# Kernel tuning notes

Measured on AMD Instinct MI355X. Metric: run time of the kernel, lower is better.

The kernel has to match this reference:

```python
import jax, jax.numpy as jnp
import numpy as np

IH, IW, HEADS, DIM_HEAD = 32, 32, 8, 48
N = IH * IW
SCALE = DIM_HEAD ** -0.5
EPS = 1e-5


def _relative_index():
    # static precompute of relative distance indices, shape [N, N] int32
    yy, xx = np.meshgrid(np.arange(IH), np.arange(IW), indexing='ij')
    coords = np.stack([yy.ravel(), xx.ravel()])  # [2, N]
    rel = coords[:, :, None] - coords[:, None, :]  # [2, N, N]
    dist = np.ceil(np.sqrt(rel[0] ** 2 + rel[1] ** 2)).astype(np.int32)
    return jnp.asarray(dist)

REL_INDEX = _relative_index()


def _layernorm(x, w, b):
    mu = jnp.mean(x, axis=-1, keepdims=True)
    var = jnp.var(x, axis=-1, keepdims=True)
    return (x - mu) * jax.lax.rsqrt(var + EPS) * w + b


def setup_inputs() -> dict:
    key = jax.random.key(0)
    ks = jax.random.split(key, 8)
    d, inner, hid = 384, HEADS * DIM_HEAD, 1536
    return {
        'x': jax.random.normal(ks[0], (16, IH, IW, d), jnp.float32),
        'ln1_w': jnp.ones((d,), jnp.float32),
        'ln1_b': jnp.zeros((d,), jnp.float32),
        'w_qkv': jax.random.normal(ks[1], (d, 3 * inner), jnp.float32) * (d ** -0.5),
        'bias_table': jax.random.normal(ks[2], (45, HEADS), jnp.float32) * 0.02,
        'w_out': jax.random.normal(ks[3], (inner, d), jnp.float32) * (inner ** -0.5),
        'b_out': jnp.zeros((d,), jnp.float32),
        'ln2_w': jnp.ones((d,), jnp.float32),
        'ln2_b': jnp.zeros((d,), jnp.float32),
        'w1': jax.random.normal(ks[4], (d, hid), jnp.float32) * (d ** -0.5),
        'b1': jnp.zeros((hid,), jnp.float32),
        'w2': jax.random.normal(ks[5], (hid, d), jnp.float32) * (hid ** -0.5),
        'b2': jnp.zeros((d,), jnp.float32),
    }


def reference(x, ln1_w, ln1_b, w_qkv, bias_table, w_out, b_out,
              ln2_w, ln2_b, w1, b1, w2, b2):
    b = x.shape[0]
    xt = x.reshape(b, N, -1)  # b (ih iw) c

    # --- attention branch (PreNorm) ---
    h = _layernorm(xt, ln1_w, ln1_b)
    qkv = h @ w_qkv  # [b, N, 3*inner]
    q, k, v = jnp.split(qkv, 3, axis=-1)
    q = q.reshape(b, N, HEADS, DIM_HEAD).transpose(0, 2, 1, 3)
    k = k.reshape(b, N, HEADS, DIM_HEAD).transpose(0, 2, 1, 3)
    v = v.reshape(b, N, HEADS, DIM_HEAD).transpose(0, 2, 1, 3)
    dots = jnp.einsum('bhnd,bhmd->bhnm', q, k) * SCALE
    rel_bias = bias_table[REL_INDEX]  # [N, N, heads] gather
    dots = dots + rel_bias.transpose(2, 0, 1)[None]  # [1, h, N, N]
    attn = jax.nn.softmax(dots, axis=-1)
    out = jnp.einsum('bhnm,bhmd->bhnd', attn, v)
    out = out.transpose(0, 2, 1, 3).reshape(b, N, HEADS * DIM_HEAD)
    out = out @ w_out + b_out
    xt = xt + out

    # --- FFN branch (PreNorm) ---
    h = _layernorm(xt, ln2_w, ln2_b)
    h = jax.nn.gelu(h @ w1 + b1, approximate=False) @ w2 + b2
    xt = xt + h
    return xt.reshape(x.shape)
```

## Files before the change

kernel.cpp:

```cpp
#include <hip/hip_runtime.h>
#include <hip/hip_bf16.h>
#include <math.h>

typedef __bf16 bf16;
typedef __bf16 bf16x8 __attribute__((ext_vector_type(8)));
typedef __bf16 bf16x4 __attribute__((ext_vector_type(4)));
typedef __bf16 bf16x2 __attribute__((ext_vector_type(2)));
typedef float  f32x4  __attribute__((ext_vector_type(4)));

#define D_MODEL 384
#define HID     1536
#define NSEQ    1024
#define ROWS    16384
#define HEADS   8
#define DH      48
#define SCALE   0.14433756729740643f
#define MFIX    8.0f
#define BT2_N   2016
#define KVT     4608
#define QP_BH   (NSEQ * DH)
#define KP_BH   (16 * KVT)

__device__ __forceinline__ void gload16(const void* g, void* l) {
    __builtin_amdgcn_global_load_lds((const __attribute__((address_space(1))) void*)g,
                                     (__attribute__((address_space(3))) void*)l, 16, 0, 0);
}

__device__ __forceinline__ float fast_gelu(float x) {
    float u = 0.7978845608f * fmaf(0.044715f * x * x, x, x);
    float e = __expf(2.f * u);
    float t = 1.f - 2.f * __builtin_amdgcn_rcpf(e + 1.f);
    return 0.5f * x * (1.f + t);
}

__device__ __forceinline__ void wtrans_body(const float* __restrict__ in,
                                            bf16* __restrict__ out, int K, int N,
                                            int bx, int by, float (*T)[65])
{
    const int k0 = by * 64, n0 = bx * 64;
    const int rr = threadIdx.x >> 4, rc = threadIdx.x & 15;
#pragma unroll
    for (int i = 0; i < 4; ++i) {
        float4 v = *(const float4*)(in + (size_t)(k0 + rr + i * 16) * N + n0 + rc * 4);
        T[rr + i * 16][rc * 4 + 0] = v.x;  T[rr + i * 16][rc * 4 + 1] = v.y;
        T[rr + i * 16][rc * 4 + 2] = v.z;  T[rr + i * 16][rc * 4 + 3] = v.w;
    }
    __syncthreads();
#pragma unroll
    for (int i = 0; i < 4; ++i) {
        int n = rr + i * 16, kc = rc * 4;
        bf16x4 o;
        o[0] = (bf16)T[kc + 0][n];  o[1] = (bf16)T[kc + 1][n];
        o[2] = (bf16)T[kc + 2][n];  o[3] = (bf16)T[kc + 3][n];
        *(bf16x4*)(out + (size_t)(n0 + n) * K + k0 + kc) = o;
    }
}

__device__ __forceinline__ void ln_body(const float* __restrict__ x,
                                        const float* __restrict__ w,
                                        const float* __restrict__ b,
                                        bf16* __restrict__ out, int blk)
{
    int row  = blk * 4 + ((int)threadIdx.x >> 6);
    int lane = threadIdx.x & 63;
    const float* xr = x + (size_t)row * D_MODEL;

    float2 v[3];
    float s = 0.f, ss = 0.f;
#pragma unroll
    for (int i = 0; i < 3; ++i) {
        v[i] = *(const float2*)(xr + lane * 2 + i * 128);
        s  += v[i].x + v[i].y;
        ss += v[i].x * v[i].x + v[i].y * v[i].y;
    }
#pragma unroll
    for (int off = 32; off; off >>= 1) {
        s  += __shfl_xor(s,  off);
        ss += __shfl_xor(ss, off);
    }
    float mu   = s * (1.f / D_MODEL);
    float var  = ss * (1.f / D_MODEL) - mu * mu;
    float rstd = rsqrtf(var + 1e-5f);

    bf16* orow = out + (size_t)row * D_MODEL;
#pragma unroll
    for (int i = 0; i < 3; ++i) {
        int c = lane * 2 + i * 128;
        float2 wv = *(const float2*)(w + c);
        float2 bv = *(const float2*)(b + c);
        bf16x2 o;
        o[0] = (bf16)((v[i].x - mu) * rstd * wv.x + bv.x);
        o[1] = (bf16)((v[i].y - mu) * rstd * wv.y + bv.y);
        *(bf16x2*)(orow + c) = o;
    }
}

__global__ __launch_bounds__(256)
void prep_kernel(const float* __restrict__ w_qkv, const float* __restrict__ w_out,
                 const float* __restrict__ w1, const float* __restrict__ w2,
                 bf16* __restrict__ wqkvT, bf16* __restrict__ woutT,
                 bf16* __restrict__ w1T, bf16* __restrict__ w2T,
                 bf16* __restrict__ Kp, bf16* __restrict__ Vp,
                 const float* __restrict__ bias_table, float* __restrict__ Btab,
                 const float* __restrict__ x, const float* __restrict__ ln1_w,
                 const float* __restrict__ ln1_b, bf16* __restrict__ regB)
{
    __shared__ float T[64][65];
    const int bid = blockIdx.x, tid = threadIdx.x;

    if (bid < 432) {
        const float* in; bf16* outp; int K, N, nx, local;
        if (bid < 108)      { in = w_qkv; outp = wqkvT; K = 384;  N = 1152; local = bid;       nx = 18; }
        else if (bid < 144) { in = w_out; outp = woutT; K = 384;  N = 384;  local = bid - 108; nx = 6;  }
        else if (bid < 288) { in = w1;    outp = w1T;   K = 384;  N = 1536; local = bid - 144; nx = 24; }
        else                { in = w2;    outp = w2T;   K = 1536; N = 384;  local = bid - 288; nx = 6;  }
        wtrans_body(in, outp, K, N, local % nx, local / nx, T);
    } else if (bid < 1072) {
        const int pb = bid - 432;
        if (pb < 512) {
            int row = pb * 256 + tid;
            bf16x8 z = {};
            bf16* p = Kp + (size_t)row * 72 + 48;
            *(bf16x8*)(p) = z;  *(bf16x8*)(p + 8) = z;  *(bf16x8*)(p + 16) = z;
        } else {
            int idx = (pb - 512) * 256 + tid;
            int tile = idx >> 4, rr = idx & 15;
            bf16 o = (bf16)1.f;
            bf16x8 ones = {o, o, o, o, o, o, o, o};
            bf16* p = Vp + (size_t)tile * KVT + (48 + rr) * 72;
#pragma unroll
            for (int c = 0; c < 9; ++c) *(bf16x8*)(p + c * 8) = ones;
        }
    } else if (bid < 1080) {
        int idx = (bid - 1072) * 256 + tid;
        if (idx < BT2_N) {
            int dy = idx / 63, dx = idx % 63 - 31;
            int s2 = dy * dy + dx * dx;
            int r = (int)ceilf(sqrtf((float)s2));
            while (r * r < s2) ++r;
            while (r > 0 && (r - 1) * (r - 1) >= s2) --r;
#pragma unroll
            for (int h = 0; h < HEADS; ++h)
                Btab[h * BT2_N + idx] = bias_table[r * HEADS + h] - MFIX;
        }
    } else {
        ln_body(x, ln1_w, ln1_b, regB, bid - 1080);
    }
}

__global__ __launch_bounds__(256)
void ln_kernel(const float* __restrict__ x, const float* __restrict__ w,
               const float* __restrict__ b, bf16* __restrict__ out)
{
    ln_body(x, w, b, out, blockIdx.x);
}

template<int EPI, typename CT>
__global__ __launch_bounds__(256)
void gemm3_kernel(const bf16* __restrict__ A, const bf16* __restrict__ BT,
                  CT* __restrict__ C, const float* __restrict__ bias,
                  const float* __restrict__ res, int nxblk, int Nn, int K,
                  bf16* __restrict__ qp, bf16* __restrict__ kp, bf16* __restrict__ vp)
{
    __shared__ alignas(16) bf16 As[128][64];
    __shared__ alignas(16) bf16 Bs[128][64];

    const int bid  = blockIdx.x;
    const int xcd  = bid & 7;
    const int slot = bid >> 3;
    const int yy   = slot / nxblk;
    const int m0   = (yy * 8 + xcd) * 128;
    const int n0   = (slot - yy * nxblk) * 128;

    const int tid  = threadIdx.x;
    const int w    = tid >> 6;
    const int lane = tid & 63;
    const int quad = lane >> 4;
    const int l16  = lane & 15;

    const int srow = lane >> 3;
    const int scol = (lane & 7) * 8;

    f32x4 acc[4][4] = {};

    for (int kt = 0; kt < K; kt += 64) {
        __syncthreads();
#pragma unroll
        for (int c = 0; c < 4; ++c) {
            const int ch = w * 4 + c;
            gload16(A  + (size_t)(m0 + ch * 8 + srow) * K + kt + scol, &As[ch * 8][0]);
            gload16(BT + (size_t)(n0 + ch * 8 + srow) * K + kt + scol, &Bs[ch * 8][0]);
        }
        __syncthreads();

#pragma unroll
        for (int kk = 0; kk < 2; ++kk) {
            bf16x8 af[4], bfr[4];
#pragma unroll
            for (int mt = 0; mt < 4; ++mt)
                af[mt] = *(const bf16x8*)(&As[(w & 1) * 64 + mt * 16 + l16][kk * 32 + quad * 8]);
#pragma unroll
            for (int nt = 0; nt < 4; ++nt)
                bfr[nt] = *(const bf16x8*)(&Bs[(w >> 1) * 64 + nt * 16 + l16][kk * 32 + quad * 8]);
#pragma unroll
            for (int mt = 0; mt < 4; ++mt)
#pragma unroll
                for (int nt = 0; nt < 4; ++nt)
                    acc[mt][nt] = __builtin_amdgcn_mfma_f32_16x16x32_bf16(
                        af[mt], bfr[nt], acc[mt][nt], 0, 0, 0);
        }
    }

#pragma unroll
    for (int mt = 0; mt < 4; ++mt) {
#pragma unroll
        for (int nt = 0; nt < 4; ++nt) {
            const int c0 = n0 + (w >> 1) * 64 + nt * 16;
            const int c  = c0 + l16;
            float bi = (EPI == 1 || EPI == 2) ? bias[c] : 0.f;
#pragma unroll
            for (int r = 0; r < 4; ++r) {
                int row = m0 + (w & 1) * 64 + mt * 16 + quad * 4 + r;
                float v = acc[mt][nt][r] + bi;
                if (EPI == 1) {
                    v += res[(size_t)row * Nn + c];
                    C[(size_t)row * Nn + c] = (CT)v;
                } else if (EPI == 2) {
                    v = fast_gelu(v);
                    C[(size_t)row * Nn + c] = (CT)v;
                } else {
                    int b   = row >> 10, seq = row & 1023;
                    if (c0 < 384) {
                        int h = c / 48, d = c - h * 48;
                        qp[(size_t)(b * 8 + h) * QP_BH + seq * 48 + d] = (bf16)(v * SCALE);
                    } else if (c0 < 768) {
                        int ck = c - 384;
                        int h = ck / 48, d = ck - h * 48;
                        kp[(size_t)(b * 8 + h) * KP_BH + (seq >> 6) * KVT
                           + (seq & 63) * 72 + d] = (bf16)v;
                    } else {
                        int cv = c - 768;
                        int h = cv / 48, d = cv - h * 48;
                        vp[(size_t)(b * 8 + h) * KP_BH + (seq >> 6) * KVT
                           + d * 72 + (seq & 63)] = (bf16)v;
                    }
                }
            }
        }
    }
}

__global__ __launch_bounds__(512)
void attn_kernel(const bf16* __restrict__ Qp, const bf16* __restrict__ Kp,
                 const bf16* __restrict__ Vp, const float* __restrict__ Btab,
                 bf16* __restrict__ out)
{
    __shared__ alignas(16) bf16 Ks[2][64][72];
    __shared__ alignas(16) bf16 Vs[2][64][72];
    __shared__ alignas(16) bf16 Ps[8][2][16][72];
    __shared__ alignas(16) float B2f[BT2_N];

    const int bid  = blockIdx.x;
    const int xcd  = bid & 7;
    const int slot = bid >> 3;
    const int qc   = slot & 3;
    const int bh   = (slot >> 2) * 8 + xcd;
    const int q0   = qc * 256;
    const int tid  = threadIdx.x;
    const int wave = tid >> 6;
    const int lane = tid & 63;
    const int quad = lane >> 4;
    const int l16  = lane & 15;
    const int b    = bh >> 3, h = bh & 7;

    {
        const char* src = (const char*)(Btab + (size_t)h * BT2_N);
        int off = tid * 16;
        if (off < BT2_N * 4)
            gload16(src + off, (char*)B2f + wave * 1024);
    }

    bf16x8 qf0[2], qf1[2];
    int qy[2], qxp[2];
#pragma unroll
    for (int s = 0; s < 2; ++s) {
        int qrow = q0 + s * 128 + wave * 16 + l16;
        const bf16* qptr = Qp + (size_t)bh * QP_BH + qrow * 48;
        qf0[s] = *(const bf16x8*)(qptr + quad * 8);
#pragma unroll
        for (int c = 0; c < 8; ++c) qf1[s][c] = (bf16)0.f;
        if (quad < 2) qf1[s] = *(const bf16x8*)(qptr + 32 + quad * 8);
        qy[s]  = qrow >> 5;
        qxp[s] = (qrow & 31) + 31;
    }

    f32x4 o_acc[2][4] = {};

    auto STAGE = [&](int tt, int bufsel) {
        if (wave < 6) {
            const bf16* kb = Kp + (size_t)(bh * 16 + tt) * KVT;
            const bf16* vb = Vp + (size_t)(bh * 16 + tt) * KVT;
#pragma unroll
            for (int j = 0; j < 3; ++j) {
                int i = wave * 3 + j;
                if (i < 9) gload16(kb + i * 512 + lane * 8,
                                   (bf16*)&Ks[bufsel][0][0] + i * 512);
                else       gload16(vb + (i - 9) * 512 + lane * 8,
                                   (bf16*)&Vs[bufsel][0][0] + (i - 9) * 512);
            }
        }
    };

    STAGE(0, 0);

    for (int t = 0; t < 16; ++t) {
        const int cur = t & 1;
        if (t < 15) {
            STAGE(t + 1, cur ^ 1);
            asm volatile("s_waitcnt vmcnt(3)" ::: "memory");
        } else {
            asm volatile("s_waitcnt vmcnt(0)" ::: "memory");
        }
        __builtin_amdgcn_s_barrier();
        __builtin_amdgcn_sched_barrier(0);

        const int n0 = t * 64;

        f32x4 sa[2][4] = {};
#pragma unroll
        for (int nt = 0; nt < 4; ++nt) {
            bf16x8 a0 = *(const bf16x8*)(&Ks[cur][nt * 16 + l16][quad * 8]);
            bf16x8 a1 = *(const bf16x8*)(&Ks[cur][nt * 16 + l16][32 + quad * 8]);
#pragma unroll
            for (int s = 0; s < 2; ++s) {
                sa[s][nt] = __builtin_amdgcn_mfma_f32_16x16x32_bf16(a0, qf0[s], sa[s][nt], 0, 0, 0);
                sa[s][nt] = __builtin_amdgcn_mfma_f32_16x16x32_bf16(a1, qf1[s], sa[s][nt], 0, 0, 0);
            }
        }

#pragma unroll
        for (int s = 0; s < 2; ++s)
#pragma unroll
            for (int nt = 0; nt < 4; ++nt) {
                const int j0 = n0 + nt * 16 + quad * 4;
                int dy  = qy[s] - (j0 >> 5);
                int iay = dy < 0 ? -dy : dy;
                const int ib0 = iay * 63 + qxp[s] - (j0 & 31);
                bf16x4 pk;
#pragma unroll
                for (int r = 0; r < 4; ++r)
                    pk[r] = (bf16)__expf(sa[s][nt][r] + B2f[ib0 - r]);
                *(bf16x4*)(&Ps[wave][s][l16][nt * 16 + quad * 4]) = pk;
            }

#pragma unroll
        for (int kk = 0; kk < 2; ++kk) {
            bf16x8 vf[4];
#pragma unroll
            for (int d = 0; d < 4; ++d)
                vf[d] = *(const bf16x8*)(&Vs[cur][d * 16 + l16][kk * 32 + quad * 8]);
#pragma unroll
            for (int s = 0; s < 2; ++s) {
                bf16x8 pf = *(const bf16x8*)(&Ps[wave][s][l16][kk * 32 + quad * 8]);
#pragma unroll
                for (int d = 0; d < 4; ++d)
                    o_acc[s][d] = __builtin_amdgcn_mfma_f32_16x16x32_bf16(
                        pf, vf[d], o_acc[s][d], 0, 0, 0);
            }
        }

        __builtin_amdgcn_s_barrier();
    }

#pragma unroll
    for (int s = 0; s < 2; ++s)
#pragma unroll
        for (int r = 0; r < 4; ++r) {
            float inv = 1.f / o_acc[s][3][r];
            int row = q0 + s * 128 + wave * 16 + quad * 4 + r;
            bf16* orow = out + ((size_t)b * NSEQ + row) * D_MODEL + h * DH;
#pragma unroll
            for (int d = 0; d < 3; ++d)
                orow[d * 16 + l16] = (bf16)(o_acc[s][d][r] * inv);
        }
}

extern "C" void kernel_launch(void* const* d_in, const int* in_sizes, int n_in,
                              void* d_out, int out_size, void* d_ws, size_t ws_size,
                              hipStream_t stream)
{
    const float* x          = (const float*)d_in[0];
    const float* ln1_w      = (const float*)d_in[1];
    const float* ln1_b      = (const float*)d_in[2];
    const float* w_qkv      = (const float*)d_in[3];
    const float* bias_table = (const float*)d_in[4];
    const float* w_out      = (const float*)d_in[5];
    const float* b_out      = (const float*)d_in[6];
    const float* ln2_w      = (const float*)d_in[7];
    const float* ln2_b      = (const float*)d_in[8];
    const float* w1         = (const float*)d_in[9];
    const float* b1         = (const float*)d_in[10];
    const float* w2         = (const float*)d_in[11];
    const float* b2         = (const float*)d_in[12];
    float* out = (float*)d_out;

    bf16* regA  = (bf16*)d_ws;
    bf16* Qpack = regA;
    bf16* Kpack = regA + 6291456;
    bf16* Vpack = regA + 15728640;
    bf16* regB  = regA + (size_t)ROWS * HID;
    bf16* wqkvT = regB + (size_t)ROWS * D_MODEL;
    bf16* woutT = wqkvT + 1152 * 384;
    bf16* w1T   = woutT + 384 * 384;
    bf16* w2T   = w1T + 1536 * 384;
    float* Btab = (float*)(w2T + 384 * 1536);
    float* x1   = out;

    prep_kernel<<<5176, 256, 0, stream>>>(
        w_qkv, w_out, w1, w2, wqkvT, woutT, w1T, w2T,
        Kpack, Vpack, bias_table, Btab, x, ln1_w, ln1_b, regB);
    gemm3_kernel<3, bf16><<<(1152 / 128) * (ROWS / 128), 256, 0, stream>>>(
        regB, wqkvT, (bf16*)nullptr, nullptr, nullptr, 1152 / 128, 1152, D_MODEL,
        Qpack, Kpack, Vpack);
    attn_kernel<<<512, 512, 0, stream>>>(Qpack, Kpack, Vpack, Btab, regB);
    gemm3_kernel<1, float><<<(D_MODEL / 128) * (ROWS / 128), 256, 0, stream>>>(
        regB, woutT, x1, b_out, x, D_MODEL / 128, D_MODEL, D_MODEL,
        nullptr, nullptr, nullptr);
    ln_kernel<<<ROWS / 4, 256, 0, stream>>>(x1, ln2_w, ln2_b, regB);
    gemm3_kernel<2, bf16><<<(HID / 128) * (ROWS / 128), 256, 0, stream>>>(
        regB, w1T, regA, b1, nullptr, HID / 128, HID, D_MODEL,
        nullptr, nullptr, nullptr);
    gemm3_kernel<1, float><<<(D_MODEL / 128) * (ROWS / 128), 256, 0, stream>>>(
        regA, w2T, out, b2, x1, D_MODEL / 128, D_MODEL, HID,
        nullptr, nullptr, nullptr);
}
```

Measured before the change: 312.4 us.

## Double-buffer LDS tiles in GEMM to overlap global loads with MFMA

The GEMM kernel now keeps two LDS stages for the A and B tiles. It issues the next K-tile's global-to-LDS loads before computing on the current tile, using s_waitcnt vmcnt(8) so only the older stage must have landed. This is meant to hide global memory latency behind the MFMA work instead of stalling on two full barriers per iteration. In exchange, LDS use doubles to 64KB per block, which may lower occupancy, and correctness depends on the hand-placed waitcnt and barriers.

```diff
diff --git a/kernel.cpp b/kernel.cpp
--- a/kernel.cpp
+++ b/kernel.cpp
@@ -162,8 +162,8 @@
                   const float* __restrict__ res, int nxblk, int Nn, int K,
                   bf16* __restrict__ qp, bf16* __restrict__ kp, bf16* __restrict__ vp)
 {
-    __shared__ alignas(16) bf16 As[128][64];
-    __shared__ alignas(16) bf16 Bs[128][64];
+    __shared__ alignas(16) bf16 As[2][128][64];
+    __shared__ alignas(16) bf16 Bs[2][128][64];
 
     const int bid  = blockIdx.x;
     const int xcd  = bid & 7;
@@ -182,26 +182,41 @@
     const int scol = (lane & 7) * 8;
 
     f32x4 acc[4][4] = {};
-
-    for (int kt = 0; kt < K; kt += 64) {
-        __syncthreads();
+    const int nst = K >> 6;
+
+    auto STAGE = [&](int tt, int bufsel) {
 #pragma unroll
         for (int c = 0; c < 4; ++c) {
             const int ch = w * 4 + c;
-            gload16(A  + (size_t)(m0 + ch * 8 + srow) * K + kt + scol, &As[ch * 8][0]);
-            gload16(BT + (size_t)(n0 + ch * 8 + srow) * K + kt + scol, &Bs[ch * 8][0]);
-        }
-        __syncthreads();
+            gload16(A  + (size_t)(m0 + ch * 8 + srow) * K + tt * 64 + scol,
+                    &As[bufsel][ch * 8][0]);
+            gload16(BT + (size_t)(n0 + ch * 8 + srow) * K + tt * 64 + scol,
+                    &Bs[bufsel][ch * 8][0]);
+        }
+    };
+
+    STAGE(0, 0);
+
+    for (int t = 0; t < nst; ++t) {
+        const int cur = t & 1;
+        if (t + 1 < nst) {
+            STAGE(t + 1, cur ^ 1);
+            asm volatile("s_waitcnt vmcnt(8)" ::: "memory");
+        } else {
+            asm volatile("s_waitcnt vmcnt(0)" ::: "memory");
+        }
+        __builtin_amdgcn_s_barrier();
+        __builtin_amdgcn_sched_barrier(0);
 
 #pragma unroll
         for (int kk = 0; kk < 2; ++kk) {
             bf16x8 af[4], bfr[4];
 #pragma unroll
             for (int mt = 0; mt < 4; ++mt)
-                af[mt] = *(const bf16x8*)(&As[(w & 1) * 64 + mt * 16 + l16][kk * 32 + quad * 8]);
+                af[mt] = *(const bf16x8*)(&As[cur][(w & 1) * 64 + mt * 16 + l16][kk * 32 + quad * 8]);
 #pragma unroll
             for (int nt = 0; nt < 4; ++nt)
-                bfr[nt] = *(const bf16x8*)(&Bs[(w >> 1) * 64 + nt * 16 + l16][kk * 32 + quad * 8]);
+                bfr[nt] = *(const bf16x8*)(&Bs[cur][(w >> 1) * 64 + nt * 16 + l16][kk * 32 + quad * 8]);
 #pragma unroll
             for (int mt = 0; mt < 4; ++mt)
 #pragma unroll
@@ -209,6 +224,8 @@
                     acc[mt][nt] = __builtin_amdgcn_mfma_f32_16x16x32_bf16(
                         af[mt], bfr[nt], acc[mt][nt], 0, 0, 0);
         }
+
+        __builtin_amdgcn_s_barrier();
     }
 
 #pragma unroll
```

Result: faster. 298.0 us (-4.6%).
